# Optimization experiments

Measured on AMD Instinct MI355X. Metric: run time of the kernel, lower is better.

The kernel has to match this reference:

```python
import jax, jax.numpy as jnp
import numpy as np

MAP_W = 500
INTERP_H, INTERP_W = 1024, 2048


def _bilinear_ac(x, out_h, out_w):
    # torch F.interpolate(mode='bilinear', align_corners=True), separable
    N, C, H, W = x.shape
    ys = jnp.linspace(0.0, H - 1, out_h)
    y0 = jnp.floor(ys).astype(jnp.int32)
    y1 = jnp.minimum(y0 + 1, H - 1)
    wy = (ys - y0.astype(x.dtype))[None, None, :, None]
    rows = x[:, :, y0, :] * (1 - wy) + x[:, :, y1, :] * wy  # (N,C,out_h,W)
    xs = jnp.linspace(0.0, W - 1, out_w)
    x0 = jnp.floor(xs).astype(jnp.int32)
    x1 = jnp.minimum(x0 + 1, W - 1)
    wx = (xs - x0.astype(x.dtype))[None, None, None, :]
    return rows[:, :, :, x0] * (1 - wx) + rows[:, :, :, x1] * wx


def _conv(x, w, pad):
    return jax.lax.conv_general_dilated(x, w, (1, 1), [(pad, pad), (pad, pad)],
                                        dimension_numbers=('NCHW', 'OIHW', 'NCHW'))


def _bn_relu(x, g, b):
    # BatchNorm2d in training mode: biased batch stats over (N,H,W)
    mu = jnp.mean(x, axis=(0, 2, 3), keepdims=True)
    var = jnp.var(x, axis=(0, 2, 3), keepdims=True)
    xn = (x - mu) * jax.lax.rsqrt(var + 1e-5)
    return jax.nn.relu(xn * g[None, :, None, None] + b[None, :, None, None])


def setup_inputs() -> dict:
    key = jax.random.key(0)
    ks = jax.random.split(key, 24)
    C, NOBJ = 64, 21
    features = jax.random.normal(ks[0], (1, 1, C, 256, 512), dtype=jnp.float32)
    proj_indices = jax.random.randint(ks[1], (1, MAP_W * MAP_W), 0, 400000, dtype=jnp.int64)
    masks_inliers = jax.random.bernoulli(ks[2], 0.5, (1, INTERP_H, INTERP_W))
    rgb_no_norm = jax.random.uniform(ks[3], (1, INTERP_H, INTERP_W, 3), dtype=jnp.float32) * 255.0
    def cw(k, o, i, kh, kw):
        return jax.random.normal(k, (o, i, kh, kw), dtype=jnp.float32) * (1.0 / np.sqrt(i * kh * kw))
    return {
        'features': features, 'proj_indices': proj_indices,
        'masks_inliers': masks_inliers, 'rgb_no_norm': rgb_no_norm,
        'w1': cw(ks[4], 128, C, 7, 7), 'g1': jnp.ones(128), 'b1': jnp.zeros(128),
        'w2': cw(ks[5], 64, 128, 3, 3), 'g2': jnp.ones(64), 'b2': jnp.zeros(64),
        'w3': cw(ks[6], 48, 64, 3, 3), 'g3': jnp.ones(48), 'b3': jnp.zeros(48),
        'w4': cw(ks[7], 48, 48, 3, 3), 'g4': jnp.ones(48), 'b4': jnp.zeros(48),
        'w5': cw(ks[8], NOBJ, 48, 1, 1), 'b5': jnp.zeros(NOBJ),
    }


def reference(features, proj_indices, masks_inliers, rgb_no_norm,
              w1, g1, b1, w2, g2, b2, w3, g3, b3, w4, g4, b4, w5, b5):
    N, T, C, H, W = features.shape  # N = 1
    feat = _bilinear_ac(features[:, 0], INTERP_H, INTERP_W)      # (N,C,1024,2048)
    feat = feat.transpose(0, 2, 3, 1).reshape(-1, C)             # row-major NHWC flatten
    rgb_flat = rgb_no_norm.reshape(-1, 3)
    mask_flat = masks_inliers.reshape(-1)
    # stable compaction: inlier pixels first, in original row-major order
    # (equivalent to torch boolean-mask gather feature[mask_inliers, :])
    order = jnp.argsort((~mask_flat).astype(jnp.int32), stable=True)
    compact_f = feat[order]
    compact_rgb = rgb_flat[order]
    idx = proj_indices.reshape(-1)
    m = idx < jnp.max(idx)                                       # sentinel = max value
    state = jnp.where(m[:, None], compact_f[idx], 0.0)           # replace-mode scatter
    state_rgb = jnp.where(m[:, None], compact_rgb[idx], 0.0)
    rgb_write = state_rgb.reshape(MAP_W, MAP_W, 3)
    observed_masks = m.reshape(N, MAP_W, MAP_W)
    memory = state.reshape(N, MAP_W, MAP_W, C).transpose(0, 3, 1, 2)
    # decoder (first conv in_channels fixed to C to match memory)
    x = _bn_relu(_conv(memory, w1, 3), g1, b1)
    x = _bn_relu(_conv(x, w2, 1), g2, b2)
    x = _bn_relu(_conv(x, w3, 1), g3, b3)
    x = _bn_relu(_conv(x, w4, 1), g4, b4)
    semmap = _conv(x, w5, 0) + b5[None, :, None, None]
    return (semmap, observed_masks, rgb_write)
```

## Files before the change

### kernel.cpp

```cpp
#include <hip/hip_runtime.h>

#define MAPN 250000
#define NPIX 2097152

typedef unsigned short ushort_t;
typedef __attribute__((ext_vector_type(4))) float f32x4;

__device__ inline ushort_t f2bf(float f){
  unsigned u = __float_as_uint(f);
  u = (u + 0x7fffu + ((u >> 16) & 1u)) >> 16;
  return (ushort_t)u;
}
__device__ inline float bf2f(ushort_t h){ return __uint_as_float(((unsigned)h) << 16); }

__device__ __forceinline__ void glds16(const void* g, void* l){
  __builtin_amdgcn_global_load_lds((const __attribute__((address_space(1))) unsigned int*)g,
                                   (__attribute__((address_space(3))) unsigned int*)l, 16, 0, 0);
}

__device__ inline int read_mask(const void* p, int i, int t){
  if (t==0) return ((const int*)p)[i] != 0;
  if (t==1) return ((const unsigned char*)p)[i] != 0;
  if (t==3) return ((const long long*)p)[i] != 0;
  return ((const float*)p)[i] != 0.0f;
}
__device__ inline int read_idx(const void* p, int i, int t){
  if (t==1) return (int)((const long long*)p)[i];
  return ((const int*)p)[i];
}

__global__ void detect_kernel(const int* __restrict__ mask_w, const int* __restrict__ idx_w,
                              int* __restrict__ flags, int* __restrict__ maxidx){
  int tid = threadIdx.x;
  int orv=0, modd=0, inz=0;
  for (int i=tid;i<4096;i+=256) orv |= mask_w[i];
  for (int i=tid;i<2048;i+=256) modd += (mask_w[2*i+1]!=0);
  for (int i=tid;i<2048;i+=256) inz  += (idx_w[2*i+1]!=0);
  __shared__ int sOr[256], sM[256], sI[256];
  sOr[tid]=orv; sM[tid]=modd; sI[tid]=inz; __syncthreads();
  for (int o=128;o;o>>=1){ if(tid<o){ sOr[tid]|=sOr[tid+o]; sM[tid]+=sM[tid+o]; sI[tid]+=sI[tid+o]; } __syncthreads(); }
  if (tid==0){
    int o = sOr[0];
    int mt;
    if ((o & ~1) == 0)               mt = (sM[0] > 0) ? 0 : 3;
    else if ((o & ~0x01010101) == 0) mt = 1;
    else                             mt = 2;
    flags[0] = mt;
    flags[1] = (sI[0] > 0) ? 0 : 1;
    maxidx[0] = 0;
  }
}

__global__ void feat_transpose(const float* __restrict__ f, ushort_t* __restrict__ out){
  __shared__ float tile[64][65];
  int tid = threadIdx.x;
  int y = blockIdx.y;
  int x0 = blockIdx.x * 64;
  #pragma unroll
  for (int pass=0; pass<16; pass++){
    int c = pass*4 + (tid>>6);
    int x = x0 + (tid & 63);
    tile[c][tid & 63] = f[(size_t)c*131072 + (size_t)y*512 + x];
  }
  __syncthreads();
  #pragma unroll
  for (int pass=0; pass<16; pass++){
    int xl = pass*4 + (tid>>6);
    int c  = tid & 63;
    out[((size_t)y*512 + x0 + xl)*64 + c] = f2bf(tile[c][xl]);
  }
}

__global__ void scan_count(const void* __restrict__ mask, const int* __restrict__ flags,
                           int* __restrict__ blkSums){
  int t = flags[0];
  int tid = threadIdx.x;
  int base = blockIdx.x*1024 + tid*4;
  int s = 0;
  #pragma unroll
  for (int j=0;j<4;j++) s += read_mask(mask, base+j, t);
  __shared__ int red[256];
  red[tid] = s; __syncthreads();
  for (int o=128;o;o>>=1){ if (tid<o) red[tid]+=red[tid+o]; __syncthreads(); }
  if (tid==0) blkSums[blockIdx.x] = red[0];
}

__global__ void scan_offsets(const int* __restrict__ blkSums, int* __restrict__ blkOffs){
  __shared__ int tsum[256];
  int tid = threadIdx.x;
  int loc[8]; int s=0;
  #pragma unroll
  for (int j=0;j<8;j++){ loc[j]=blkSums[tid*8+j]; s+=loc[j]; }
  tsum[tid]=s; __syncthreads();
  for (int o=1;o<256;o<<=1){
    int v = (tid>=o)? tsum[tid-o] : 0;
    __syncthreads();
    tsum[tid] += v;
    __syncthreads();
  }
  int run = tsum[tid]-s;
  #pragma unroll
  for (int j=0;j<8;j++){ blkOffs[tid*8+j]=run; run+=loc[j]; }
  if (tid==255) blkOffs[2048]=run;
}

__global__ void build_table(const void* __restrict__ mask, const int* __restrict__ flags,
                            const int* __restrict__ blkOffs, int* __restrict__ table){
  int t = flags[0];
  int tid = threadIdx.x;
  int base = blockIdx.x*1024 + tid*4;
  int mv[4]; int s=0;
  #pragma unroll
  for (int j=0;j<4;j++){ mv[j]=read_mask(mask, base+j, t); s+=mv[j]; }
  __shared__ int red[256];
  red[tid]=s; __syncthreads();
  for (int o=1;o<256;o<<=1){
    int v = (tid>=o)? red[tid-o] : 0;
    __syncthreads();
    red[tid]+=v;
    __syncthreads();
  }
  int excl = red[tid]-s + blkOffs[blockIdx.x];
  int total = blkOffs[2048];
  #pragma unroll
  for (int j=0;j<4;j++){
    int p = base+j;
    int pos;
    if (mv[j]){ pos = excl; excl++; }
    else      { pos = total + (p - excl); }
    table[pos] = p;
  }
}

__global__ void max_idx_kernel(const void* __restrict__ idxp, const int* __restrict__ flags,
                               int* __restrict__ mx){
  int t = flags[1];
  int m = 0;
  for (int i = blockIdx.x*blockDim.x + threadIdx.x; i < MAPN; i += gridDim.x*blockDim.x)
    m = max(m, read_idx(idxp, i, t));
  #pragma unroll
  for (int o=32;o;o>>=1) m = max(m, __shfl_down(m, o));
  if ((threadIdx.x & 63) == 0) atomicMax(mx, m);
}

__global__ void gather_kernel(const void* __restrict__ idxp, const int* __restrict__ flags,
                              const int* __restrict__ mxp, const int* __restrict__ table,
                              const ushort_t* __restrict__ Fhwc, const float* __restrict__ rgb,
                              unsigned char* __restrict__ mem_f8, float* __restrict__ out_obs,
                              float* __restrict__ out_rgb){
  int cell = blockIdx.x*4 + (threadIdx.x>>6);
  int lane = threadIdx.x & 63;
  int t = flags[1];
  int mx = *mxp;
  int idx = read_idx(idxp, cell, t);
  bool m = idx < mx;
  float v = 0.0f, r = 0.0f;
  if (m){
    int p = table[idx];
    int py = p >> 11, px = p & 2047;
    float fy = py * (255.0f/1023.0f);
    int y0 = (int)fy; float wy = fy - (float)y0; int y1 = min(y0+1, 255);
    float fx = px * (511.0f/2047.0f);
    int x0 = (int)fx; float wx = fx - (float)x0; int x1 = min(x0+1, 511);
    const ushort_t* f00 = Fhwc + ((size_t)y0*512 + x0)*64;
    const ushort_t* f01 = Fhwc + ((size_t)y0*512 + x1)*64;
    const ushort_t* f10 = Fhwc + ((size_t)y1*512 + x0)*64;
    const ushort_t* f11 = Fhwc + ((size_t)y1*512 + x1)*64;
    float w00=(1.0f-wy)*(1.0f-wx), w01=(1.0f-wy)*wx, w10=wy*(1.0f-wx), w11=wy*wx;
    v = w00*bf2f(f00[lane]) + w01*bf2f(f01[lane]) + w10*bf2f(f10[lane]) + w11*bf2f(f11[lane]);
    if (lane < 3) r = rgb[(size_t)p*3 + lane];
  }
  int q = __builtin_amdgcn_cvt_pk_fp8_f32(v, 0.0f, 0, false);
  mem_f8[(size_t)cell*64 + lane] = (unsigned char)(q & 0xff);
  if (lane == 0) out_obs[cell] = m ? 1.0f : 0.0f;
  if (lane < 3)  out_rgb[(size_t)cell*3 + lane] = r;
}

__global__ void wprep_f8(const float* __restrict__ w, unsigned char* __restrict__ out,
                         int O, int I, int CIPAD, int KK){
  int co = blockIdx.x;
  int n = KK*CIPAD;
  int NFS = (O+15)>>4;
  int KC  = CIPAD>>5;
  float mx = 0.f;
  for (int e=threadIdx.x; e<n; e+=256){
    int ci = e % CIPAD;
    if (ci < I){
      int t = e / CIPAD;
      mx = fmaxf(mx, fabsf(w[((size_t)co*I + ci)*KK + t]));
    }
  }
  __shared__ float red[256];
  red[threadIdx.x]=mx; __syncthreads();
  for (int o=128;o;o>>=1){ if(threadIdx.x<o) red[threadIdx.x]=fmaxf(red[threadIdx.x],red[threadIdx.x+o]); __syncthreads(); }
  float m = red[0];
  float sc = (m > 0.f) ? exp2f(floorf(log2f(224.0f/m))) : 1.0f;
  for (int e=threadIdx.x; e<n; e+=256){
    int t = e / CIPAD, ci = e % CIPAD;
    float v = (ci < I) ? w[((size_t)co*I + ci)*KK + t]*sc : 0.0f;
    int q = __builtin_amdgcn_cvt_pk_fp8_f32(v, 0.0f, 0, false);
    int kc = ci>>5, g=(ci>>3)&3, j=ci&7;
    int l = g*16 + (co&15);
    size_t pos = ((size_t)(t*KC + kc)*NFS + (co>>4))*512 + l*8 + j;
    out[pos] = (unsigned char)(q & 0xff);
  }
}

template<int CI, int CO, int COPAD, int KS, int PAD, bool HASBN, int CIREAL,
         int TR, int WM, int WN>
__global__ __launch_bounds__(256, 2) void conv2d_f8(const void* __restrict__ in,
                                                    const unsigned char* __restrict__ wt,
                                                    const float* __restrict__ scsh,
                                                    ushort_t* __restrict__ out,
                                                    float* __restrict__ partials){
  constexpr int TCOL = 64;
  constexpr int ECOL = TCOL + 2*PAD;
  constexpr int E    = TR*ECOL;
  constexpr int MF   = TR*4;
  constexpr int MI   = MF/WM;
  constexpr int NFS  = CO/16;
  constexpr int NFW  = NFS/WN;
  constexpr int KC   = CI/32;
  constexpr int CIG  = CI/8;
  constexpr int TB   = CO*CI;
  constexpr int NSL  = TB/1024;
  constexpr int NT   = KS*KS;
  constexpr int TOT  = E*CIG;
  constexpr int PASSES = (TOT+255)/256;
  constexpr int SCN = HASBN ? CIREAL : 1;

  __shared__ unsigned char sA[E*CI + 128];
  __shared__ unsigned char sB[2][TB];
  __shared__ float sStat[4][NFW][16][2];
  __shared__ float sSc[SCN], sSh[SCN];

  const int tid = threadIdx.x, lane = tid & 63, wv = tid >> 6;
  const int wm = wv / WN, wn = wv % WN;
  const int cc = blockIdx.x & 7;
  const int rb = blockIdx.x >> 3;
  const int x0 = cc*TCOL, yb = rb*TR;

  const ushort_t* inb = (const ushort_t*)in;
  const unsigned char* in8 = (const unsigned char*)in;

  if (HASBN){
    for (int i=tid;i<CIREAL;i+=256){ sSc[i]=scsh[i]; sSh[i]=scsh[CIREAL+i]; }
    __syncthreads();
  }

  int ebase[MI], frow[MI], fcolb[MI];
  #pragma unroll
  for (int mi=0;mi<MI;mi++){
    int f = wm*MI + mi;
    frow[mi]  = f >> 2;
    fcolb[mi] = (f & 3) * 16;
    ebase[mi] = frow[mi]*ECOL + fcolb[mi] + (lane & 15);
  }

  f32x4 acc[MI][NFW];
  #pragma unroll
  for (int mi=0;mi<MI;mi++)
    #pragma unroll
    for (int ni=0;ni<NFW;ni++) acc[mi][ni] = (f32x4)0.0f;

  for (int s=wv; s<NSL; s+=4)
    glds16((const char*)wt + (size_t)s*1024 + lane*16, &sB[0][s*1024]);

  int cur = 0;

  for (int kh=0; kh<KS; kh++){
    #pragma unroll
    for (int i=0;i<PASSES;i++){
      int c = i*256 + tid;
      if ((TOT % 256 == 0) || c < TOT){
        int e = c / CIG, ci8 = (c % CIG)*8;
        int row = e / ECOL, col = e % ECOL;
        int yy = yb + row + kh - PAD;
        int xx = x0 + col - PAD;
        uint2 q = make_uint2(0u,0u);
        bool ok = ((unsigned)yy < 500u) && ((unsigned)xx < 500u) && (!HASBN || ci8 < CIREAL);
        if (ok){
          if (HASBN){
            uint4 v = *(const uint4*)(inb + ((size_t)yy*500 + xx)*CI + ci8);
            ushort_t* hv = (ushort_t*)&v;
            float f[8];
            #pragma unroll
            for (int j=0;j<8;j++)
              f[j] = fmaxf(fmaf(bf2f(hv[j]), sSc[ci8+j], sSh[ci8+j]), 0.0f);
            int d0 = __builtin_amdgcn_cvt_pk_fp8_f32(f[0], f[1], 0, false);
            d0     = __builtin_amdgcn_cvt_pk_fp8_f32(f[2], f[3], d0, true);
            int d1 = __builtin_amdgcn_cvt_pk_fp8_f32(f[4], f[5], 0, false);
            d1     = __builtin_amdgcn_cvt_pk_fp8_f32(f[6], f[7], d1, true);
            q = make_uint2((unsigned)d0, (unsigned)d1);
          } else {
            q = *(const uint2*)(in8 + ((size_t)yy*500 + xx)*CI + ci8);
          }
        }
        unsigned wa = ((unsigned)(e*CI + ci8)) ^ ((unsigned)(e&15)<<3);
        *(uint2*)(sA + wa) = q;
      }
    }
    __syncthreads();

    for (int kw=0; kw<KS; kw++){
      int t = kh*KS + kw;
      if (t+1 < NT){
        for (int s=wv; s<NSL; s+=4)
          glds16((const char*)wt + (size_t)(t+1)*TB + (size_t)s*1024 + lane*16,
                 &sB[cur^1][s*1024]);
      }
      #pragma unroll
      for (int kc=0;kc<KC;kc++){
        long long bfr[NFW];
        #pragma unroll
        for (int ni=0;ni<NFW;ni++)
          bfr[ni] = *(const long long*)(&sB[cur][((kc*NFS + wn*NFW + ni)<<9) + lane*8]);
        #pragma unroll
        for (int mi=0;mi<MI;mi++){
          int e = ebase[mi] + kw;
          unsigned ra = ((unsigned)(e*CI + kc*32 + (lane>>4)*8)) ^ ((unsigned)(e&15)<<3);
          long long af = *(const long long*)(sA + ra);
          #pragma unroll
          for (int ni=0;ni<NFW;ni++)
            acc[mi][ni] = __builtin_amdgcn_mfma_f32_16x16x32_fp8_fp8(af, bfr[ni], acc[mi][ni], 0,0,0);
        }
      }
      __syncthreads();
      cur ^= 1;
    }
  }

  #pragma unroll
  for (int ni=0;ni<NFW;ni++){
    float ps=0.f, pq=0.f;
    #pragma unroll
    for (int mi=0;mi<MI;mi++){
      int colb = fcolb[mi] + (lane>>4)*4;
      size_t rowoff = (size_t)(yb + frow[mi])*500;
      #pragma unroll
      for (int j=0;j<4;j++){
        float v = acc[mi][ni][j];
        int colAbs = x0 + colb + j;
        if (colAbs < 500){
          ps += v; pq += v*v;
          out[(rowoff + colAbs)*COPAD + wn*(NFW*16) + ni*16 + (lane&15)] = f2bf(v);
        }
      }
    }
    ps += __shfl_xor(ps, 16); pq += __shfl_xor(pq, 16);
    ps += __shfl_xor(ps, 32); pq += __shfl_xor(pq, 32);
    if (lane < 16){ sStat[wv][ni][lane][0]=ps; sStat[wv][ni][lane][1]=pq; }
  }
  __syncthreads();
  if (tid < CO){
    int wn_ = tid / (NFW*16);
    int r = tid % (NFW*16);
    int ni_ = r >> 4, col = r & 15;
    float s = 0.f, q = 0.f;
    #pragma unroll
    for (int m=0;m<WM;m++){
      s += sStat[m*WN + wn_][ni_][col][0];
      q += sStat[m*WN + wn_][ni_][col][1];
    }
    partials[(size_t)blockIdx.x*(2*CO) + tid]      = s;
    partials[(size_t)blockIdx.x*(2*CO) + CO + tid] = q;
  }
}

__global__ void bn_reduce2(const float* __restrict__ partials, int nblk, int CO,
                           const float* __restrict__ g, const float* __restrict__ b,
                           float* __restrict__ scsh){
  int c = blockIdx.x;
  float s=0.f, q=0.f;
  for (int i=threadIdx.x; i<nblk; i+=256){
    s += partials[(size_t)i*(2*CO) + c];
    q += partials[(size_t)i*(2*CO) + CO + c];
  }
  __shared__ float rs[256], rq[256];
  rs[threadIdx.x]=s; rq[threadIdx.x]=q; __syncthreads();
  for (int o=128;o;o>>=1){
    if (threadIdx.x<o){ rs[threadIdx.x]+=rs[threadIdx.x+o]; rq[threadIdx.x]+=rq[threadIdx.x+o]; }
    __syncthreads();
  }
  if (threadIdx.x==0){
    float mean = rs[0]*(1.0f/(float)MAPN);
    float var  = rq[0]*(1.0f/(float)MAPN) - mean*mean;
    float inv  = rsqrtf(var + 1e-5f);
    float sc   = g[c]*inv;
    scsh[c]    = sc;
    scsh[CO+c] = b[c] - mean*sc;
  }
}

__global__ void conv5_kernel(const ushort_t* __restrict__ in, const float* __restrict__ w,
                             const float* __restrict__ bias, const float* __restrict__ scsh,
                             float* __restrict__ out){
  __shared__ float sw[21*48];
  __shared__ float sb[21];
  __shared__ float sc[48], sh[48];
  for (int i=threadIdx.x;i<1008;i+=256) sw[i]=w[i];
  if (threadIdx.x<21) sb[threadIdx.x]=bias[threadIdx.x];
  if (threadIdx.x<48){ sc[threadIdx.x]=scsh[threadIdx.x]; sh[threadIdx.x]=scsh[48+threadIdx.x]; }
  __syncthreads();
  int pix = blockIdx.x*256 + threadIdx.x;
  if (pix >= MAPN) return;
  float acc[21];
  #pragma unroll
  for (int i=0;i<21;i++) acc[i]=0.0f;
  const ushort_t* ip = in + (size_t)pix*64;
  #pragma unroll
  for (int cg=0; cg<6; cg++){
    uint4 v = *(const uint4*)(ip + cg*8);
    ushort_t* hv = (ushort_t*)&v;
    #pragma unroll
    for (int j=0;j<8;j++){
      int ci = cg*8+j;
      float s = fmaxf(fmaf(bf2f(hv[j]), sc[ci], sh[ci]), 0.0f);
      #pragma unroll
      for (int co=0;co<21;co++) acc[co]=fmaf(s, sw[co*48+ci], acc[co]);
    }
  }
  #pragma unroll
  for (int co=0;co<21;co++) out[(size_t)co*MAPN + pix] = acc[co] + sb[co];
}

static inline size_t al256(size_t x){ return (x + 255) & ~(size_t)255; }

extern "C" void kernel_launch(void* const* d_in, const int* in_sizes, int n_in,
                              void* d_out, int out_size, void* d_ws, size_t ws_size,
                              hipStream_t stream){
  const float* features = (const float*)d_in[0];
  const void*  proj     = d_in[1];
  const void*  mask     = d_in[2];
  const float* rgb      = (const float*)d_in[3];
  const float* w1 = (const float*)d_in[4];
  const float* g1 = (const float*)d_in[5];
  const float* b1 = (const float*)d_in[6];
  const float* w2 = (const float*)d_in[7];
  const float* g2 = (const float*)d_in[8];
  const float* b2 = (const float*)d_in[9];
  const float* w3 = (const float*)d_in[10];
  const float* g3 = (const float*)d_in[11];
  const float* b3 = (const float*)d_in[12];
  const float* w4 = (const float*)d_in[13];
  const float* g4 = (const float*)d_in[14];
  const float* b4 = (const float*)d_in[15];
  const float* w5 = (const float*)d_in[16];
  const float* b5 = (const float*)d_in[17];

  char* ws = (char*)d_ws;
  size_t off = 0;
  unsigned char* mem_f8 = (unsigned char*)(ws + off); off += al256((size_t)MAPN*64);
  ushort_t* actA   = (ushort_t*)(ws + off); off += al256((size_t)MAPN*128*2);
  ushort_t* actB   = (ushort_t*)(ws + off); off += al256((size_t)MAPN*64*2);
  ushort_t* Fhwc   = (ushort_t*)(ws + off); off += al256((size_t)131072*64*2);
  int*      table  = (int*)(ws + off);      off += al256((size_t)NPIX*4);
  unsigned char* wh1 = (unsigned char*)(ws + off); off += al256((size_t)49*2*8*512);
  unsigned char* wh2 = (unsigned char*)(ws + off); off += al256((size_t)9*4*4*512);
  unsigned char* wh3 = (unsigned char*)(ws + off); off += al256((size_t)9*2*3*512);
  unsigned char* wh4 = (unsigned char*)(ws + off); off += al256((size_t)9*2*3*512);
  float*    partials = (float*)(ws + off);  off += al256((size_t)2048*256*4);
  int* blkSums = (int*)(ws + off); off += al256(2048*4);
  int* blkOffs = (int*)(ws + off); off += al256(2049*4);
  int* maxidx  = (int*)(ws + off); off += 256;
  int* flags   = (int*)(ws + off); off += 256;
  float* scsh1 = (float*)(ws + off); off += al256(256*4);
  float* scsh2 = (float*)(ws + off); off += al256(256*4);
  float* scsh3 = (float*)(ws + off); off += al256(256*4);
  float* scsh4 = (float*)(ws + off); off += al256(256*4);

  float* out_sem = (float*)d_out;
  float* out_obs = out_sem + (size_t)21*MAPN;
  float* out_rgb = out_obs + MAPN;

  detect_kernel<<<1,256,0,stream>>>((const int*)mask, (const int*)proj, flags, maxidx);
  feat_transpose<<<dim3(8,256),256,0,stream>>>(features, Fhwc);

  scan_count<<<2048,256,0,stream>>>(mask, flags, blkSums);
  scan_offsets<<<1,256,0,stream>>>(blkSums, blkOffs);
  build_table<<<2048,256,0,stream>>>(mask, flags, blkOffs, table);

  max_idx_kernel<<<256,256,0,stream>>>(proj, flags, maxidx);

  wprep_f8<<<128,256,0,stream>>>(w1, wh1, 128, 64, 64, 49);
  wprep_f8<<<64,256,0,stream>>>(w2, wh2, 64, 128, 128, 9);
  wprep_f8<<<48,256,0,stream>>>(w3, wh3, 48, 64, 64, 9);
  wprep_f8<<<48,256,0,stream>>>(w4, wh4, 48, 48, 64, 9);

  gather_kernel<<<62500,256,0,stream>>>(proj, flags, maxidx, table, Fhwc, rgb,
                                        mem_f8, out_obs, out_rgb);

  conv2d_f8<64,128,128,7,3,false,64,4,2,2><<<125*8,256,0,stream>>>(mem_f8, wh1, nullptr, actA, partials);
  bn_reduce2<<<128,256,0,stream>>>(partials, 1000, 128, g1, b1, scsh1);

  conv2d_f8<128,64,64,3,1,true,128,4,2,2><<<125*8,256,0,stream>>>(actA, wh2, scsh1, actB, partials);
  bn_reduce2<<<64,256,0,stream>>>(partials, 1000, 64, g2, b2, scsh2);

  conv2d_f8<64,48,64,3,1,true,64,4,4,1><<<125*8,256,0,stream>>>(actB, wh3, scsh2, actA, partials);
  bn_reduce2<<<48,256,0,stream>>>(partials, 1000, 48, g3, b3, scsh3);

  conv2d_f8<64,48,64,3,1,true,48,4,4,1><<<125*8,256,0,stream>>>(actA, wh4, scsh3, actB, partials);
  bn_reduce2<<<48,256,0,stream>>>(partials, 1000, 48, g4, b4, scsh4);

  conv5_kernel<<<(MAPN+255)/256,256,0,stream>>>(actB, w5, b5, scsh4, out_sem);
}
```

Measured before the change: 505.0 us.

## Load conv weight fragments directly into registers, drop LDS weight staging

Weight fragments now go straight from global memory into registers, double-buffered in two register arrays, instead of being staged into a shared-memory double buffer with global_load_lds. Each tap's weights are prefetched while the previous tap computes, and the per-tap __syncthreads is removed, leaving one barrier per kernel row. This frees LDS (better occupancy) and cuts barriers and LDS reads. The cost is more registers, plus repeated global/L2 weight loads by every wave that L1 cache must absorb.

```diff
diff --git a/kernel.cpp b/kernel.cpp
--- a/kernel.cpp
+++ b/kernel.cpp
@@ -12,11 +12,6 @@
   return (ushort_t)u;
 }
 __device__ inline float bf2f(ushort_t h){ return __uint_as_float(((unsigned)h) << 16); }
-
-__device__ __forceinline__ void glds16(const void* g, void* l){
-  __builtin_amdgcn_global_load_lds((const __attribute__((address_space(1))) unsigned int*)g,
-                                   (__attribute__((address_space(3))) unsigned int*)l, 16, 0, 0);
-}
 
 __device__ inline int read_mask(const void* p, int i, int t){
   if (t==0) return ((const int*)p)[i] != 0;
@@ -222,15 +217,13 @@
   constexpr int NFW  = NFS/WN;
   constexpr int KC   = CI/32;
   constexpr int CIG  = CI/8;
-  constexpr int TB   = CO*CI;
-  constexpr int NSL  = TB/1024;
   constexpr int NT   = KS*KS;
   constexpr int TOT  = E*CIG;
   constexpr int PASSES = (TOT+255)/256;
   constexpr int SCN = HASBN ? CIREAL : 1;
+  constexpr int NB  = KC*NFW;
 
   __shared__ unsigned char sA[E*CI + 128];
-  __shared__ unsigned char sB[2][TB];
   __shared__ float sStat[4][NFW][16][2];
   __shared__ float sSc[SCN], sSh[SCN];
 
@@ -242,6 +235,7 @@
 
   const ushort_t* inb = (const ushort_t*)in;
   const unsigned char* in8 = (const unsigned char*)in;
+  const unsigned char* wlane = wt + (lane<<3);
 
   if (HASBN){
     for (int i=tid;i<CIREAL;i+=256){ sSc[i]=scsh[i]; sSh[i]=scsh[CIREAL+i]; }
@@ -263,10 +257,32 @@
     #pragma unroll
     for (int ni=0;ni<NFW;ni++) acc[mi][ni] = (f32x4)0.0f;
 
-  for (int s=wv; s<NSL; s+=4)
-    glds16((const char*)wt + (size_t)s*1024 + lane*16, &sB[0][s*1024]);
-
-  int cur = 0;
+  long long bA[NB], bB[NB];
+
+  auto loadB = [&](int t, long long* dst){
+    #pragma unroll
+    for (int kc=0;kc<KC;kc++)
+      #pragma unroll
+      for (int ni=0;ni<NFW;ni++)
+        dst[kc*NFW+ni] = *(const long long*)(wlane +
+            ((size_t)((t*KC + kc)*NFS + wn*NFW + ni) << 9));
+  };
+  auto computeTap = [&](int kw, const long long* b){
+    #pragma unroll
+    for (int kc=0;kc<KC;kc++){
+      #pragma unroll
+      for (int mi=0;mi<MI;mi++){
+        int e = ebase[mi] + kw;
+        unsigned ra = ((unsigned)(e*CI + kc*32 + (lane>>4)*8)) ^ ((unsigned)(e&15)<<3);
+        long long af = *(const long long*)(sA + ra);
+        #pragma unroll
+        for (int ni=0;ni<NFW;ni++)
+          acc[mi][ni] = __builtin_amdgcn_mfma_f32_16x16x32_fp8_fp8(af, b[kc*NFW+ni], acc[mi][ni], 0,0,0);
+      }
+    }
+  };
+
+  loadB(0, bA);
 
   for (int kh=0; kh<KS; kh++){
     #pragma unroll
@@ -302,32 +318,25 @@
     }
     __syncthreads();
 
-    for (int kw=0; kw<KS; kw++){
+    int kw = 0;
+    #pragma unroll
+    for (int p=0; p<KS/2; p++){
       int t = kh*KS + kw;
-      if (t+1 < NT){
-        for (int s=wv; s<NSL; s+=4)
-          glds16((const char*)wt + (size_t)(t+1)*TB + (size_t)s*1024 + lane*16,
-                 &sB[cur^1][s*1024]);
-      }
+      if (t+1 < NT) loadB(t+1, bB);
+      computeTap(kw, bA);
+      kw++;
+      if (t+2 < NT) loadB(t+2, bA);
+      computeTap(kw, bB);
+      kw++;
+    }
+    {
+      int t = kh*KS + kw;
+      if (t+1 < NT) loadB(t+1, bB);
+      computeTap(kw, bA);
       #pragma unroll
-      for (int kc=0;kc<KC;kc++){
-        long long bfr[NFW];
-        #pragma unroll
-        for (int ni=0;ni<NFW;ni++)
-          bfr[ni] = *(const long long*)(&sB[cur][((kc*NFS + wn*NFW + ni)<<9) + lane*8]);
-        #pragma unroll
-        for (int mi=0;mi<MI;mi++){
-          int e = ebase[mi] + kw;
-          unsigned ra = ((unsigned)(e*CI + kc*32 + (lane>>4)*8)) ^ ((unsigned)(e&15)<<3);
-          long long af = *(const long long*)(sA + ra);
-          #pragma unroll
-          for (int ni=0;ni<NFW;ni++)
-            acc[mi][ni] = __builtin_amdgcn_mfma_f32_16x16x32_fp8_fp8(af, bfr[ni], acc[mi][ni], 0,0,0);
-        }
-      }
-      __syncthreads();
-      cur ^= 1;
-    }
+      for (int i=0;i<NB;i++) bA[i] = bB[i];
+    }
+    __syncthreads();
   }
 
   #pragma unroll
```

New measurement: 843.0 us. 66.9% more time.

## Prefetch conv weight taps two ahead with 4-deep LDS ring and vmcnt waits

Applied to the files above, without the earlier changes.

Replaces the double-buffered weight tile with a four-slot LDS ring that prefetches the weights for tap t+2 while tap t computes. The full __syncthreads after each tap becomes a targeted s_waitcnt vmcnt plus a raw s_barrier, so only the tile about to be used has to have landed. The goal is to hide global-to-LDS weight latency behind the MFMA work and cut barrier cost. In exchange, LDS use for weights doubles, which may limit occupancy, and the hand-written waitcnt counts depend on each wave issuing a fixed number of loads.

```diff
diff --git a/kernel.cpp b/kernel.cpp
--- a/kernel.cpp
+++ b/kernel.cpp
@@ -16,6 +16,13 @@
 __device__ __forceinline__ void glds16(const void* g, void* l){
   __builtin_amdgcn_global_load_lds((const __attribute__((address_space(1))) unsigned int*)g,
                                    (__attribute__((address_space(3))) unsigned int*)l, 16, 0, 0);
+}
+
+template<int N> __device__ __forceinline__ void waitv(){
+  if constexpr (N >= 4)      asm volatile("s_waitcnt vmcnt(4)" ::: "memory");
+  else if constexpr (N == 2) asm volatile("s_waitcnt vmcnt(2)" ::: "memory");
+  else                       asm volatile("s_waitcnt vmcnt(0)" ::: "memory");
+  __builtin_amdgcn_sched_barrier(0);
 }
 
 __device__ inline int read_mask(const void* p, int i, int t){
@@ -224,13 +231,14 @@
   constexpr int CIG  = CI/8;
   constexpr int TB   = CO*CI;
   constexpr int NSL  = TB/1024;
+  constexpr int GPW  = (NSL+3)/4;
   constexpr int NT   = KS*KS;
   constexpr int TOT  = E*CIG;
   constexpr int PASSES = (TOT+255)/256;
   constexpr int SCN = HASBN ? CIREAL : 1;
 
   __shared__ unsigned char sA[E*CI + 128];
-  __shared__ unsigned char sB[2][TB];
+  __shared__ unsigned char sB[4][TB];
   __shared__ float sStat[4][NFW][16][2];
   __shared__ float sSc[SCN], sSh[SCN];
 
@@ -263,12 +271,16 @@
     #pragma unroll
     for (int ni=0;ni<NFW;ni++) acc[mi][ni] = (f32x4)0.0f;
 
+  #pragma unroll
   for (int s=wv; s<NSL; s+=4)
     glds16((const char*)wt + (size_t)s*1024 + lane*16, &sB[0][s*1024]);
-
-  int cur = 0;
+  #pragma unroll
+  for (int s=wv; s<NSL; s+=4)
+    glds16((const char*)wt + (size_t)TB + (size_t)s*1024 + lane*16, &sB[1][s*1024]);
 
   for (int kh=0; kh<KS; kh++){
+    __builtin_amdgcn_s_barrier();
+    __builtin_amdgcn_sched_barrier(0);
     #pragma unroll
     for (int i=0;i<PASSES;i++){
       int c = i*256 + tid;
@@ -300,21 +312,33 @@
         *(uint2*)(sA + wa) = q;
       }
     }
-    __syncthreads();
-
+    asm volatile("s_waitcnt lgkmcnt(0)" ::: "memory");
+    __builtin_amdgcn_sched_barrier(0);
+    __builtin_amdgcn_s_barrier();
+    __builtin_amdgcn_sched_barrier(0);
+
+    #pragma unroll
     for (int kw=0; kw<KS; kw++){
       int t = kh*KS + kw;
-      if (t+1 < NT){
+      if (t + 2 < NT){
+        unsigned char* dst = sB[(t+2)&3];
+        const char* src = (const char*)wt + (size_t)(t+2)*TB;
+        #pragma unroll
         for (int s=wv; s<NSL; s+=4)
-          glds16((const char*)wt + (size_t)(t+1)*TB + (size_t)s*1024 + lane*16,
-                 &sB[cur^1][s*1024]);
+          glds16(src + (size_t)s*1024 + lane*16, dst + s*1024);
+        waitv<2*GPW>();
+      } else {
+        waitv<0>();
       }
+      __builtin_amdgcn_s_barrier();
+      __builtin_amdgcn_sched_barrier(0);
+      const unsigned char* bb = sB[t&3];
       #pragma unroll
       for (int kc=0;kc<KC;kc++){
         long long bfr[NFW];
         #pragma unroll
         for (int ni=0;ni<NFW;ni++)
-          bfr[ni] = *(const long long*)(&sB[cur][((kc*NFS + wn*NFW + ni)<<9) + lane*8]);
+          bfr[ni] = *(const long long*)(bb + (((kc*NFS + wn*NFW + ni)<<9) + lane*8));
         #pragma unroll
         for (int mi=0;mi<MI;mi++){
           int e = ebase[mi] + kw;
@@ -325,10 +349,9 @@
             acc[mi][ni] = __builtin_amdgcn_mfma_f32_16x16x32_fp8_fp8(af, bfr[ni], acc[mi][ni], 0,0,0);
         }
       }
-      __syncthreads();
-      cur ^= 1;
     }
   }
+  __syncthreads();
 
   #pragma unroll
   for (int ni=0;ni<NFW;ni++){
```

Result: slower. 956.8 us (+89.5%).
